# Kernel tuning notes

Hardware: AMD Instinct MI355X
Metric: run time of the kernel (lower is better)

The kernel has to match this reference:

```python
import jax, jax.numpy as jnp
import numpy as np

BIG = 1e30  # stands in for sys.maxsize in fp32-safe form


def _find_neg_anchors(e_actv, host):
    # Full pairwise Euclidean distance matrix (equivalent to the
    # pdist -> triangular reconstruction in the torch code).
    sq = jnp.sum(e_actv * e_actv, axis=1)                       # [n]
    d2 = sq[:, None] + sq[None, :] - 2.0 * (e_actv @ e_actv.T)  # [n, n]
    dist = jnp.sqrt(jnp.maximum(d2, 0.0))
    n = e_actv.shape[0]
    # mask: self (diagonal) and same-discriminator pairs -> huge distance
    same_discr = host[:, None] == host[None, :]
    eye = jnp.eye(n, dtype=bool)
    dist = jnp.where(same_discr | eye, BIG, dist)
    idxs = jnp.argmin(dist, axis=1)                             # [n]
    return e_actv[idxs]                                         # gather


def setup_inputs() -> dict:
    key = jax.random.key(0)
    k1, k2, k3 = jax.random.split(key, 3)
    n, d = 8192, 256
    e_actv = jax.random.normal(k1, (n, d), dtype=jnp.float32)
    e_ap = jax.random.normal(k2, (n, d), dtype=jnp.float32)
    host = jax.random.randint(k3, (n,), 0, 64, dtype=jnp.int64 if jax.config.read('jax_enable_x64') else jnp.int32)
    return {"e_actv": e_actv, "e_ap": e_ap, "host": host}


def reference(e_actv, e_ap, host):
    # forward returns (e_actv, e_ap, e_an); e_an computed under no_grad
    e_an = jax.lax.stop_gradient(_find_neg_anchors(e_actv, host))
    return (e_actv, e_ap, e_an)
```

## Files before the change

### kernel.cpp

```cpp
#include <hip/hip_runtime.h>
#include <hip/hip_bf16.h>
#include <cmath>
#include <cstddef>

#define N 8192
#define D 256
#define BI 128
#define KT 32
#define NT (N / BI)
#define NTRI (NT * (NT + 1) / 2)

typedef __attribute__((ext_vector_type(8))) short short8;
typedef __attribute__((ext_vector_type(4))) float float4v;

__device__ inline ushort f2bf(float x) {
    __hip_bfloat16 h = __float2bfloat16(x);
    return __builtin_bit_cast(ushort, h);
}
__device__ inline float bf2f(ushort u) {
    __hip_bfloat16 h = __builtin_bit_cast(__hip_bfloat16, u);
    return __bfloat162float(h);
}

__device__ inline void gl_lds16(const void* g, void* l) {
    __builtin_amdgcn_global_load_lds(
        (const __attribute__((address_space(1))) void*)g,
        (__attribute__((address_space(3))) void*)l,
        16, 0, 0);
}

__device__ inline unsigned long long packKI(float k, int idx) {
    unsigned u = __float_as_uint(k);
    u = (u & 0x80000000u) ? ~u : (u | 0x80000000u);
    return ((unsigned long long)u << 32) | (unsigned)idx;
}

__device__ inline int triT(int t) { return t * (129 - t) / 2; }

__global__ void prep_kernel(const float4* __restrict__ a, const float4* __restrict__ p,
                            float4* __restrict__ out, float* __restrict__ sq,
                            ushort4* __restrict__ hi, ushort4* __restrict__ lo,
                            unsigned long long* __restrict__ M) {
    const int gsz = gridDim.x * blockDim.x;
    const int g0 = blockIdx.x * blockDim.x + threadIdx.x;
    const int total = N * D / 4;

    for (int idx = g0; idx < total; idx += gsz) {
        float4 v = a[idx];
        out[idx] = v;
        ushort4 h, l;
        h.x = f2bf(v.x); l.x = f2bf(v.x - bf2f(h.x));
        h.y = f2bf(v.y); l.y = f2bf(v.y - bf2f(h.y));
        h.z = f2bf(v.z); l.z = f2bf(v.z - bf2f(h.z));
        h.w = f2bf(v.w); l.w = f2bf(v.w - bf2f(h.w));
        hi[idx] = h; lo[idx] = l;
        float s = v.x * v.x + v.y * v.y + v.z * v.z + v.w * v.w;
        #pragma unroll
        for (int off = 32; off; off >>= 1) s += __shfl_down(s, off);
        if ((threadIdx.x & 63) == 0) sq[idx >> 6] = s;
    }
    for (int idx = g0; idx < total; idx += gsz) out[total + idx] = p[idx];
    for (int i = g0; i < N; i += gsz) M[i] = 0xFFFFFFFFFFFFFFFFull;
}

__launch_bounds__(256)
__global__ void argmin_sym(const ushort* __restrict__ Ehi, const ushort* __restrict__ Elo,
                           const int* __restrict__ host, const float* __restrict__ sq,
                           unsigned long long* __restrict__ M) {
    const int b = blockIdx.x;
    int ti = (int)floor(64.5 - sqrt(64.5 * 64.5 - 2.0 * (double)b));
    while (triT(ti + 1) <= b) ti++;
    while (triT(ti) > b) ti--;
    const int tj = ti + (b - triT(ti));

    __shared__ __align__(16) ushort lds[4 * BI * KT];
    __shared__ float sqA_s[BI], sqB_s[BI];
    __shared__ int   hostB_s[BI];
    ushort* Ahi_s = lds;
    ushort* Alo_s = lds + 1 * BI * KT;
    ushort* Bhi_s = lds + 2 * BI * KT;
    ushort* Blo_s = lds + 3 * BI * KT;

    const int ib0 = ti * BI;
    const int jb0 = tj * BI;
    const int tid = threadIdx.x;
    const int lane = tid & 63;
    const int wave = tid >> 6;
    const int wrow = wave >> 1;
    const int wcol = wave & 1;
    const int tx = lane & 15;
    const int q  = lane >> 4;

    unsigned hostAp[4];
    #pragma unroll
    for (int rt = 0; rt < 4; rt++) {
        unsigned p = 0;
        #pragma unroll
        for (int reg = 0; reg < 4; reg++) {
            int hv = host[ib0 + wrow * 64 + rt * 16 + q * 4 + reg];
            p |= ((unsigned)hv & 0xFFu) << (8 * reg);
        }
        hostAp[rt] = p;
    }

    float4v acc[4][4];
    #pragma unroll
    for (int rt = 0; rt < 4; rt++)
        #pragma unroll
        for (int ct = 0; ct < 4; ct++) acc[rt][ct] = (float4v)(0.0f);

    for (int kt = 0; kt < D; kt += KT) {
        __syncthreads();
        #pragma unroll
        for (int t = 0; t < 2; t++) {
            int f = tid + t * 256;
            int row = f >> 2;
            int c = f & 3;
            size_t gA = (size_t)(ib0 + row) * D + kt + c * 8;
            size_t gB = (size_t)(jb0 + row) * D + kt + c * 8;
            int o = f * 8;
            gl_lds16(&Ehi[gA], &Ahi_s[o]);
            gl_lds16(&Elo[gA], &Alo_s[o]);
            gl_lds16(&Ehi[gB], &Bhi_s[o]);
            gl_lds16(&Elo[gB], &Blo_s[o]);
        }
        if (kt == 0 && tid < BI) {
            sqA_s[tid] = sq[ib0 + tid];
            sqB_s[tid] = sq[jb0 + tid];
            hostB_s[tid] = host[jb0 + tid];
        }
        __syncthreads();

        short8 ah[4], al[4], bh[4], bl[4];
        #pragma unroll
        for (int rt = 0; rt < 4; rt++) {
            int o = (wrow * 64 + rt * 16 + tx) * KT + q * 8;
            ah[rt] = *(const short8*)&Ahi_s[o];
            al[rt] = *(const short8*)&Alo_s[o];
        }
        #pragma unroll
        for (int ct = 0; ct < 4; ct++) {
            int o = (wcol * 64 + ct * 16 + tx) * KT + q * 8;
            bh[ct] = *(const short8*)&Bhi_s[o];
            bl[ct] = *(const short8*)&Blo_s[o];
        }
        #pragma unroll
        for (int rt = 0; rt < 4; rt++)
            #pragma unroll
            for (int ct = 0; ct < 4; ct++)
                acc[rt][ct] = __builtin_amdgcn_mfma_f32_16x16x32_bf16(ah[rt], bh[ct], acc[rt][ct], 0, 0, 0);
        #pragma unroll
        for (int rt = 0; rt < 4; rt++)
            #pragma unroll
            for (int ct = 0; ct < 4; ct++)
                acc[rt][ct] = __builtin_amdgcn_mfma_f32_16x16x32_bf16(ah[rt], bl[ct], acc[rt][ct], 0, 0, 0);
        #pragma unroll
        for (int rt = 0; rt < 4; rt++)
            #pragma unroll
            for (int ct = 0; ct < 4; ct++)
                acc[rt][ct] = __builtin_amdgcn_mfma_f32_16x16x32_bf16(al[rt], bh[ct], acc[rt][ct], 0, 0, 0);
    }

    __syncthreads();
    float* rowV = (float*)lds;
    int*   rowI = (int*)lds + 256;
    float* colV = (float*)lds + 512;
    int*   colI = (int*)lds + 768;

    #pragma unroll
    for (int rt = 0; rt < 4; rt++) {
        unsigned hp = hostAp[rt];
        #pragma unroll
        for (int reg = 0; reg < 4; reg++) {
            int il = wrow * 64 + rt * 16 + q * 4 + reg;
            int ig = ib0 + il;
            int ha = (int)((hp >> (8 * reg)) & 0xFFu);
            float v = 3.0e38f; int ix = 0x7fffffff;
            #pragma unroll
            for (int ct = 0; ct < 4; ct++) {
                int jl = wcol * 64 + ct * 16 + tx;
                int jg = jb0 + jl;
                float key = sqB_s[jl] - 2.0f * acc[rt][ct][reg];
                bool masked = (hostB_s[jl] == ha) || (jg == ig);
                if (!masked && (key < v || (key == v && jg < ix))) { v = key; ix = jg; }
            }
            #pragma unroll
            for (int d = 1; d < 16; d <<= 1) {
                float ov = __shfl_xor(v, d);
                int   oi = __shfl_xor(ix, d);
                if (ov < v || (ov == v && oi < ix)) { v = ov; ix = oi; }
            }
            if (tx == 0) { rowV[il * 2 + wcol] = v; rowI[il * 2 + wcol] = ix; }
        }
    }

    if (ti != tj) {
        #pragma unroll
        for (int ct = 0; ct < 4; ct++) {
            int jl = wcol * 64 + ct * 16 + tx;
            int hb = hostB_s[jl];
            float v = 3.0e38f; int ix = 0x7fffffff;
            #pragma unroll
            for (int rt = 0; rt < 4; rt++) {
                unsigned hp = hostAp[rt];
                #pragma unroll
                for (int reg = 0; reg < 4; reg++) {
                    int il = wrow * 64 + rt * 16 + q * 4 + reg;
                    int ig = ib0 + il;
                    bool masked = ((int)((hp >> (8 * reg)) & 0xFFu) == hb);
                    float key = sqA_s[il] - 2.0f * acc[rt][ct][reg];
                    if (!masked && (key < v || (key == v && ig < ix))) { v = key; ix = ig; }
                }
            }
            #pragma unroll
            for (int d = 16; d < 64; d <<= 1) {
                float ov = __shfl_xor(v, d);
                int   oi = __shfl_xor(ix, d);
                if (ov < v || (ov == v && oi < ix)) { v = ov; ix = oi; }
            }
            if (q == 0) { colV[jl * 2 + wrow] = v; colI[jl * 2 + wrow] = ix; }
        }
    }

    __syncthreads();
    if (tid < BI) {
        float v0 = rowV[tid * 2];     int x0 = rowI[tid * 2];
        float v1 = rowV[tid * 2 + 1]; int x1 = rowI[tid * 2 + 1];
        if (v1 < v0 || (v1 == v0 && x1 < x0)) { v0 = v1; x0 = x1; }
        atomicMin(&M[ib0 + tid], packKI(v0, x0));
        if (ti != tj) {
            float w0 = colV[tid * 2];     int y0 = colI[tid * 2];
            float w1 = colV[tid * 2 + 1]; int y1 = colI[tid * 2 + 1];
            if (w1 < w0 || (w1 == w0 && y1 < y0)) { w0 = w1; y0 = y1; }
            atomicMin(&M[jb0 + tid], packKI(w0, y0));
        }
    }
}

__global__ void finalize_kernel(const unsigned long long* __restrict__ M,
                                const float* __restrict__ E, float* __restrict__ out_an) {
    int row = blockIdx.x;
    int t = threadIdx.x;
    int idx = (int)(unsigned)(M[row] & 0xFFFFFFFFull);
    float4 v = *(const float4*)&E[(size_t)idx * D + t * 4];
    *(float4*)&out_an[(size_t)row * D + t * 4] = v;
}

extern "C" void kernel_launch(void* const* d_in, const int* in_sizes, int n_in,
                              void* d_out, int out_size, void* d_ws, size_t ws_size,
                              hipStream_t stream) {
    const float* e_actv = (const float*)d_in[0];
    const float* e_ap   = (const float*)d_in[1];
    const int*   host   = (const int*)d_in[2];
    float* out = (float*)d_out;

    unsigned long long* M = (unsigned long long*)d_ws;
    float*  sq  = (float*)(M + N);
    ushort* Ehi = (ushort*)(sq + N);
    ushort* Elo = Ehi + (size_t)N * D;

    prep_kernel<<<1024, 256, 0, stream>>>(
        (const float4*)e_actv, (const float4*)e_ap, (float4*)out,
        sq, (ushort4*)Ehi, (ushort4*)Elo, M);
    argmin_sym<<<NTRI, 256, 0, stream>>>(Ehi, Elo, host, sq, M);
    finalize_kernel<<<N, 64, 0, stream>>>(M, e_actv, out + 2 * (size_t)N * D);
}
```

Measured before the change: 203.4 us.

## Pre-swizzle bf16 hi/lo operands into MFMA fragment layout and load directly from global

The prep kernel now writes the bf16 hi/lo split of the embeddings in a layout that matches the MFMA 16x16x32 fragment order, so each lane's short8 operand sits contiguously in global memory. The argmin kernel drops the LDS staging loop with its per-step barriers and instead reads the fragments straight from global (via L2/L1) inside a partially unrolled k-loop. This removes LDS traffic and synchronisation, but every wave now fetches its operands independently from global memory, so reuse across waves depends on cache hits and load latency is no longer hidden by shared-memory tiling.

```diff
diff --git a/kernel.cpp b/kernel.cpp
--- a/kernel.cpp
+++ b/kernel.cpp
@@ -6,7 +6,6 @@
 #define N 8192
 #define D 256
 #define BI 128
-#define KT 32
 #define NT (N / BI)
 #define NTRI (NT * (NT + 1) / 2)
 
@@ -20,13 +19,6 @@
 __device__ inline float bf2f(ushort u) {
     __hip_bfloat16 h = __builtin_bit_cast(__hip_bfloat16, u);
     return __bfloat162float(h);
-}
-
-__device__ inline void gl_lds16(const void* g, void* l) {
-    __builtin_amdgcn_global_load_lds(
-        (const __attribute__((address_space(1))) void*)g,
-        (__attribute__((address_space(3))) void*)l,
-        16, 0, 0);
 }
 
 __device__ inline unsigned long long packKI(float k, int idx) {
@@ -37,9 +29,10 @@
 
 __device__ inline int triT(int t) { return t * (129 - t) / 2; }
 
+
 __global__ void prep_kernel(const float4* __restrict__ a, const float4* __restrict__ p,
                             float4* __restrict__ out, float* __restrict__ sq,
-                            ushort4* __restrict__ hi, ushort4* __restrict__ lo,
+                            ushort* __restrict__ Phi, ushort* __restrict__ Plo,
                             unsigned long long* __restrict__ M) {
     const int gsz = gridDim.x * blockDim.x;
     const int g0 = blockIdx.x * blockDim.x + threadIdx.x;
@@ -48,23 +41,40 @@
     for (int idx = g0; idx < total; idx += gsz) {
         float4 v = a[idx];
         out[idx] = v;
-        ushort4 h, l;
-        h.x = f2bf(v.x); l.x = f2bf(v.x - bf2f(h.x));
-        h.y = f2bf(v.y); l.y = f2bf(v.y - bf2f(h.y));
-        h.z = f2bf(v.z); l.z = f2bf(v.z - bf2f(h.z));
-        h.w = f2bf(v.w); l.w = f2bf(v.w - bf2f(h.w));
-        hi[idx] = h; lo[idx] = l;
         float s = v.x * v.x + v.y * v.y + v.z * v.z + v.w * v.w;
         #pragma unroll
         for (int off = 32; off; off >>= 1) s += __shfl_down(s, off);
         if ((threadIdx.x & 63) == 0) sq[idx >> 6] = s;
     }
     for (int idx = g0; idx < total; idx += gsz) out[total + idx] = p[idx];
+
+    const int tot8 = N * D / 8;
+    for (int o = g0; o < tot8; o += gsz) {
+        int tx = o & 15;
+        int gc = o >> 4;
+        int c  = gc & 31;
+        int g  = gc >> 5;
+        int row = g * 16 + tx;
+        const float4* src = &a[row * 64 + c * 2];
+        float4 v0 = src[0], v1 = src[1];
+        short8 h, l;
+        float f;
+        f = v0.x; h[0] = (short)f2bf(f); l[0] = (short)f2bf(f - bf2f((ushort)h[0]));
+        f = v0.y; h[1] = (short)f2bf(f); l[1] = (short)f2bf(f - bf2f((ushort)h[1]));
+        f = v0.z; h[2] = (short)f2bf(f); l[2] = (short)f2bf(f - bf2f((ushort)h[2]));
+        f = v0.w; h[3] = (short)f2bf(f); l[3] = (short)f2bf(f - bf2f((ushort)h[3]));
+        f = v1.x; h[4] = (short)f2bf(f); l[4] = (short)f2bf(f - bf2f((ushort)h[4]));
+        f = v1.y; h[5] = (short)f2bf(f); l[5] = (short)f2bf(f - bf2f((ushort)h[5]));
+        f = v1.z; h[6] = (short)f2bf(f); l[6] = (short)f2bf(f - bf2f((ushort)h[6]));
+        f = v1.w; h[7] = (short)f2bf(f); l[7] = (short)f2bf(f - bf2f((ushort)h[7]));
+        *(short8*)&Phi[(size_t)o * 8] = h;
+        *(short8*)&Plo[(size_t)o * 8] = l;
+    }
     for (int i = g0; i < N; i += gsz) M[i] = 0xFFFFFFFFFFFFFFFFull;
 }
 
 __launch_bounds__(256)
-__global__ void argmin_sym(const ushort* __restrict__ Ehi, const ushort* __restrict__ Elo,
+__global__ void argmin_sym(const ushort* __restrict__ Phi, const ushort* __restrict__ Plo,
                            const int* __restrict__ host, const float* __restrict__ sq,
                            unsigned long long* __restrict__ M) {
     const int b = blockIdx.x;
@@ -73,13 +83,10 @@
     while (triT(ti) > b) ti--;
     const int tj = ti + (b - triT(ti));
 
-    __shared__ __align__(16) ushort lds[4 * BI * KT];
     __shared__ float sqA_s[BI], sqB_s[BI];
     __shared__ int   hostB_s[BI];
-    ushort* Ahi_s = lds;
-    ushort* Alo_s = lds + 1 * BI * KT;
-    ushort* Bhi_s = lds + 2 * BI * KT;
-    ushort* Blo_s = lds + 3 * BI * KT;
+    __shared__ float rowV[2 * BI], colV[2 * BI];
+    __shared__ int   rowI[2 * BI], colI[2 * BI];
 
     const int ib0 = ti * BI;
     const int jb0 = tj * BI;
@@ -91,6 +98,12 @@
     const int tx = lane & 15;
     const int q  = lane >> 4;
 
+    if (tid < BI) {
+        sqA_s[tid] = sq[ib0 + tid];
+        sqB_s[tid] = sq[jb0 + tid];
+        hostB_s[tid] = host[jb0 + tid];
+    }
+
     unsigned hostAp[4];
     #pragma unroll
     for (int rt = 0; rt < 4; rt++) {
@@ -102,6 +115,7 @@
         }
         hostAp[rt] = p;
     }
+    __syncthreads();
 
     float4v acc[4][4];
     #pragma unroll
@@ -109,40 +123,25 @@
         #pragma unroll
         for (int ct = 0; ct < 4; ct++) acc[rt][ct] = (float4v)(0.0f);
 
-    for (int kt = 0; kt < D; kt += KT) {
-        __syncthreads();
-        #pragma unroll
-        for (int t = 0; t < 2; t++) {
-            int f = tid + t * 256;
-            int row = f >> 2;
-            int c = f & 3;
-            size_t gA = (size_t)(ib0 + row) * D + kt + c * 8;
-            size_t gB = (size_t)(jb0 + row) * D + kt + c * 8;
-            int o = f * 8;
-            gl_lds16(&Ehi[gA], &Ahi_s[o]);
-            gl_lds16(&Elo[gA], &Alo_s[o]);
-            gl_lds16(&Ehi[gB], &Bhi_s[o]);
-            gl_lds16(&Elo[gB], &Blo_s[o]);
-        }
-        if (kt == 0 && tid < BI) {
-            sqA_s[tid] = sq[ib0 + tid];
-            sqB_s[tid] = sq[jb0 + tid];
-            hostB_s[tid] = host[jb0 + tid];
-        }
-        __syncthreads();
-
+    const int ga = (ib0 >> 4) + wrow * 4;
+    const int gb = (jb0 >> 4) + wcol * 4;
+    const int txo = tx * 8;
+
+    #pragma unroll 2
+    for (int s = 0; s < 8; s++) {
+        const int c0 = s * 4 + q;
         short8 ah[4], al[4], bh[4], bl[4];
         #pragma unroll
         for (int rt = 0; rt < 4; rt++) {
-            int o = (wrow * 64 + rt * 16 + tx) * KT + q * 8;
-            ah[rt] = *(const short8*)&Ahi_s[o];
-            al[rt] = *(const short8*)&Alo_s[o];
+            int o = ((ga + rt) * 32 + c0) * 128 + txo;
+            ah[rt] = *(const short8*)&Phi[o];
+            al[rt] = *(const short8*)&Plo[o];
         }
         #pragma unroll
         for (int ct = 0; ct < 4; ct++) {
-            int o = (wcol * 64 + ct * 16 + tx) * KT + q * 8;
-            bh[ct] = *(const short8*)&Bhi_s[o];
-            bl[ct] = *(const short8*)&Blo_s[o];
+            int o = ((gb + ct) * 32 + c0) * 128 + txo;
+            bh[ct] = *(const short8*)&Phi[o];
+            bl[ct] = *(const short8*)&Plo[o];
         }
         #pragma unroll
         for (int rt = 0; rt < 4; rt++)
@@ -160,12 +159,6 @@
             for (int ct = 0; ct < 4; ct++)
                 acc[rt][ct] = __builtin_amdgcn_mfma_f32_16x16x32_bf16(al[rt], bh[ct], acc[rt][ct], 0, 0, 0);
     }
-
-    __syncthreads();
-    float* rowV = (float*)lds;
-    int*   rowI = (int*)lds + 256;
-    float* colV = (float*)lds + 512;
-    int*   colI = (int*)lds + 768;
 
     #pragma unroll
     for (int rt = 0; rt < 4; rt++) {
@@ -256,12 +249,12 @@
 
     unsigned long long* M = (unsigned long long*)d_ws;
     float*  sq  = (float*)(M + N);
-    ushort* Ehi = (ushort*)(sq + N);
-    ushort* Elo = Ehi + (size_t)N * D;
+    ushort* Phi = (ushort*)(sq + N);
+    ushort* Plo = Phi + (size_t)N * D;
 
     prep_kernel<<<1024, 256, 0, stream>>>(
         (const float4*)e_actv, (const float4*)e_ap, (float4*)out,
-        sq, (ushort4*)Ehi, (ushort4*)Elo, M);
-    argmin_sym<<<NTRI, 256, 0, stream>>>(Ehi, Elo, host, sq, M);
+        sq, Phi, Plo, M);
+    argmin_sym<<<NTRI, 256, 0, stream>>>(Phi, Plo, host, sq, M);
     finalize_kernel<<<N, 64, 0, stream>>>(M, e_actv, out + 2 * (size_t)N * D);
 }
```

Result: slower. 213.9 us (+5.2%).
